# Performance work log

Measured on AMD Instinct MI355X. Metric: run time of the kernel, lower is better.

The kernel has to match this reference:

```python
import jax, jax.numpy as jnp
import numpy as np

B, S, D = 4, 2048, 1024
H, DK = 16, 64
NEG = -1e9


def setup_inputs() -> dict:
    key = jax.random.key(0)
    ks = jax.random.split(key, 6)
    hidden_states = jax.random.normal(ks[0], (B, S, D), dtype=jnp.float32)
    # evidence-constrained mask: causal mask plus random evidence restriction
    causal = jnp.tril(jnp.ones((S, S), dtype=bool))
    evid = jax.random.bernoulli(ks[1], 0.7, (S, S))
    allowed = causal & (evid | jnp.eye(S, dtype=bool))  # diag always allowed
    attention_mask = jnp.where(allowed, 0.0, NEG).astype(jnp.float32)
    scale = 0.02
    Wq = jax.random.normal(ks[2], (H * DK, D), dtype=jnp.float32) * scale
    Wk = jax.random.normal(ks[3], (H * DK, D), dtype=jnp.float32) * scale
    Wv = jax.random.normal(ks[4], (H * DK, D), dtype=jnp.float32) * scale
    Wo = jax.random.normal(ks[5], (D, H * DK), dtype=jnp.float32) * scale
    return {"hidden_states": hidden_states, "attention_mask": attention_mask,
            "Wq": Wq, "Wk": Wk, "Wv": Wv, "Wo": Wo}


def reference(hidden_states, attention_mask, Wq, Wk, Wv, Wo):
    b, s, _ = hidden_states.shape
    # nn.Linear(bias=False): y = x @ W.T ; reshape to (B,H,S,DK)
    def proj(x, W):
        y = jnp.einsum('bsd,ed->bse', x, W)
        return y.reshape(b, s, H, DK).transpose(0, 2, 1, 3)
    q = proj(hidden_states, Wq)
    k = proj(hidden_states, Wk)
    v = proj(hidden_states, Wv)
    logits = jnp.einsum('bhqd,bhkd->bhqk', q, k) / jnp.sqrt(jnp.float32(DK))
    logits = logits + attention_mask[None, None, :, :]
    attn = jax.nn.softmax(logits, axis=-1)
    ctx = jnp.einsum('bhqk,bhkd->bhqd', attn, v)
    ctx = ctx.transpose(0, 2, 1, 3).reshape(b, s, H * DK)
    out = jnp.einsum('bse,de->bsd', ctx, Wo)
    return out
```

## Files before the change

kernel.cpp:

```cpp
#include <hip/hip_runtime.h>
#include <hip/hip_bf16.h>
#include <math.h>

#define B_  4
#define S_  2048
#define D_  1024
#define H_  16
#define DK_ 64
#define M_  (B_*S_)
#define E_  (H_*DK_)
#define LOG2E  1.4426950408889634f
#define QSCALE 0.18033688011112042f

typedef short  bf16x8 __attribute__((ext_vector_type(8)));
typedef float  f32x4  __attribute__((ext_vector_type(4)));
typedef unsigned short u16;

__device__ __forceinline__ u16 f2b(float x) {
    __hip_bfloat16 h = __float2bfloat16(x);
    return *(u16*)&h;
}

__device__ __forceinline__ void async16(const u16* g, u16* l) {
    __builtin_amdgcn_global_load_lds(
        (const __attribute__((address_space(1))) unsigned int*)g,
        (__attribute__((address_space(3))) unsigned int*)l, 16, 0, 0);
}

#define XN8 (M_ * D_ / 8)
#define WN8 (E_ * D_ / 8)
__global__ __launch_bounds__(256)
void cvt_all(const float* __restrict__ X,
             const float* __restrict__ Wq, const float* __restrict__ Wk,
             const float* __restrict__ Wv, const float* __restrict__ Wo,
             u16* __restrict__ Xb,
             u16* __restrict__ Wqb, u16* __restrict__ Wkb,
             u16* __restrict__ Wvb, u16* __restrict__ Wob) {
    int idx = blockIdx.x * 256 + threadIdx.x;
    const float* s; u16* d; int off;
    if (idx < XN8) { s = X; d = Xb; off = idx; }
    else {
        int j = idx - XN8;
        int which = j / WN8; off = j - which * WN8;
        s = which == 0 ? Wq : which == 1 ? Wk : which == 2 ? Wv : Wo;
        d = which == 0 ? Wqb : which == 1 ? Wkb : which == 2 ? Wvb : Wob;
    }
    const float4* s4 = (const float4*)s;
    float4 a = s4[2 * off], b = s4[2 * off + 1];
    u16 o[8] = {f2b(a.x), f2b(a.y), f2b(a.z), f2b(a.w),
                f2b(b.x), f2b(b.y), f2b(b.z), f2b(b.w)};
    *(uint4*)(d + (size_t)8 * off) = *(const uint4*)o;
}

__device__ __forceinline__ void gemm_core(
    const u16* __restrict__ Ag, const u16* __restrict__ Bg, int K,
    int bm, int bn, u16* As, u16* Bs, f32x4 (&acc)[4][4])
{
    const int tid  = threadIdx.x;
    const int w    = tid >> 6, lane = tid & 63;
    const int l15  = lane & 15, quad = lane >> 4;
    const int wm   = (w >> 1) * 64, wn = (w & 1) * 64;
    const int srow = lane >> 3;
    const int sg   = (lane & 7) ^ srow;
    const int sx   = l15 & 7;

    for (int k0 = 0; k0 < K; k0 += 64) {
        __syncthreads();
        #pragma unroll
        for (int i = 0; i < 4; i++) {
            const int row = w * 32 + i * 8 + srow;
            async16(Ag + (size_t)(bm + row) * K + k0 + sg * 8,
                    As + (size_t)(w * 32 + i * 8) * 64);
            async16(Bg + (size_t)(bn + row) * K + k0 + sg * 8,
                    Bs + (size_t)(w * 32 + i * 8) * 64);
        }
        __syncthreads();

        #pragma unroll
        for (int s = 0; s < 2; s++) {
            bf16x8 af[4], bf[4];
            #pragma unroll
            for (int i = 0; i < 4; i++)
                af[i] = *(const bf16x8*)(As + (size_t)(wm + i * 16 + l15) * 64
                                            + (((s * 4 + quad) ^ sx) * 8));
            #pragma unroll
            for (int j = 0; j < 4; j++)
                bf[j] = *(const bf16x8*)(Bs + (size_t)(wn + j * 16 + l15) * 64
                                            + (((s * 4 + quad) ^ sx) * 8));
            #pragma unroll
            for (int i = 0; i < 4; i++)
                #pragma unroll
                for (int j = 0; j < 4; j++)
                    acc[i][j] = __builtin_amdgcn_mfma_f32_16x16x32_bf16(af[i], bf[j], acc[i][j], 0, 0, 0);
        }
    }
}

__global__ __launch_bounds__(256)
void gemm_qkv(const u16* __restrict__ Xb,
              const u16* __restrict__ Wqb, const u16* __restrict__ Wkb,
              const u16* __restrict__ Wvb,
              u16* __restrict__ Qm, u16* __restrict__ Km, u16* __restrict__ Vt)
{
    __shared__ u16 As[128 * 64];
    __shared__ u16 Bs[128 * 64];
    const int bm    = blockIdx.x * 128;
    const int nb    = blockIdx.y;
    const int which = nb >> 3;
    const int col0  = (nb & 7) * 128;
    const u16* Bg = which == 0 ? Wqb : which == 1 ? Wkb : Wvb;

    f32x4 acc[4][4] = {};
    gemm_core(Xb, Bg, D_, bm, col0, As, Bs, acc);

    const int tid = threadIdx.x;
    const int w   = tid >> 6, lane = tid & 63;
    const int l15 = lane & 15, quad = lane >> 4;
    const int wm  = (w >> 1) * 64, wn = (w & 1) * 64;

    if (which == 2) {
        #pragma unroll
        for (int i = 0; i < 4; i++)
            #pragma unroll
            for (int j = 0; j < 4; j++) {
                int c    = col0 + wn + j * 16 + l15;
                int tok0 = bm + wm + i * 16 + quad * 4;
                u16 pk[4] = {f2b(acc[i][j][0]), f2b(acc[i][j][1]),
                             f2b(acc[i][j][2]), f2b(acc[i][j][3])};
                size_t idx = (((size_t)((tok0 >> 11) * E_ + c)) << 11) + (tok0 & 2047);
                *(uint2*)(Vt + idx) = *(const uint2*)pk;
            }
    } else {
        u16* Cm = which == 0 ? Qm : Km;
        const float sc = which == 0 ? QSCALE : 1.0f;
        #pragma unroll
        for (int i = 0; i < 4; i++)
            #pragma unroll
            for (int j = 0; j < 4; j++)
                #pragma unroll
                for (int r = 0; r < 4; r++) {
                    int row = bm + wm + i * 16 + quad * 4 + r;
                    int c   = col0 + wn + j * 16 + l15;
                    Cm[(size_t)row * E_ + c] = f2b(acc[i][j][r] * sc);
                }
    }
}

__global__ __launch_bounds__(256)
void gemm_out(const u16* __restrict__ Cmx, const u16* __restrict__ Wob,
              float* __restrict__ out)
{
    __shared__ u16 As[128 * 64];
    __shared__ u16 Bs[128 * 64];
    const int bm = blockIdx.x * 128;
    const int bn = blockIdx.y * 128;

    f32x4 acc[4][4] = {};
    gemm_core(Cmx, Wob, E_, bm, bn, As, Bs, acc);

    const int tid = threadIdx.x;
    const int w   = tid >> 6, lane = tid & 63;
    const int l15 = lane & 15, quad = lane >> 4;
    const int wm  = (w >> 1) * 64, wn = (w & 1) * 64;
    #pragma unroll
    for (int i = 0; i < 4; i++)
        #pragma unroll
        for (int j = 0; j < 4; j++)
            #pragma unroll
            for (int r = 0; r < 4; r++)
                out[(size_t)(bm + wm + i * 16 + quad * 4 + r) * D_ + bn + wn + j * 16 + l15]
                    = acc[i][j][r];
}

__global__ __launch_bounds__(512)
void flash_attn(const u16* __restrict__ Q, const u16* __restrict__ Kc,
                const u16* __restrict__ Vt, const float* __restrict__ mask,
                u16* __restrict__ ctx)
{
    const int bh  = blockIdx.x;
    const int qt  = (gridDim.y - 1) - blockIdx.y;
    const int b   = bh >> 4, h = bh & 15;
    const int tid = threadIdx.x;
    const int w   = tid >> 6, lane = tid & 63;
    const int l15 = lane & 15, quad = lane >> 4;
    const int q0  = qt * 128;
    const int nkt = 2 * qt + 2;

    __shared__ u16 Ks[64 * 64];
    __shared__ u16 Vs[64 * 64];
    __shared__ u16 Ps[8][16 * 64];

    const u16* qb = Q + ((size_t)(b * S_ + q0 + w * 16 + l15)) * E_ + h * DK_;
    bf16x8 qf0 = *(const bf16x8*)(qb + quad * 8);
    bf16x8 qf1 = *(const bf16x8*)(qb + 32 + quad * 8);

    f32x4 acc[4] = {};
    float lsum = 0.f;

    const int sr = lane >> 3;
    const int sg = (lane & 7) ^ sr;
    const int sx = l15 & 7;
    u16* Pw = &Ps[w][0];
    const float* mpb = mask + (size_t)(q0 + w * 16 + l15) * S_ + quad * 4;

    for (int kt = 0; kt < nkt; ++kt) {
        const int k0 = kt * 64;

        float4 mk[4];
        #pragma unroll
        for (int t = 0; t < 4; t++) mk[t] = *(const float4*)(mpb + k0 + t * 16);

        __syncthreads();
        {
            const int row8 = w * 8;
            async16(Kc + ((size_t)(b * S_ + k0 + row8 + sr)) * E_ + h * DK_ + sg * 8,
                    Ks + row8 * 64);
            async16(Vt + ((size_t)(bh * DK_ + row8 + sr)) * S_ + k0 + sg * 8,
                    Vs + row8 * 64);
        }
        __syncthreads();

        f32x4 st[4] = {};
        #pragma unroll
        for (int t = 0; t < 4; t++) {
            bf16x8 kf0 = *(const bf16x8*)(Ks + (t * 16 + l15) * 64 + ((quad ^ sx) * 8));
            bf16x8 kf1 = *(const bf16x8*)(Ks + (t * 16 + l15) * 64 + (((4 + quad) ^ sx) * 8));
            st[t] = __builtin_amdgcn_mfma_f32_16x16x32_bf16(kf0, qf0, st[t], 0, 0, 0);
            st[t] = __builtin_amdgcn_mfma_f32_16x16x32_bf16(kf1, qf1, st[t], 0, 0, 0);
        }

        #pragma unroll
        for (int t = 0; t < 4; t++) {
            float p0 = exp2f(fmaf(mk[t].x, LOG2E, st[t][0]));
            float p1 = exp2f(fmaf(mk[t].y, LOG2E, st[t][1]));
            float p2 = exp2f(fmaf(mk[t].z, LOG2E, st[t][2]));
            float p3 = exp2f(fmaf(mk[t].w, LOG2E, st[t][3]));
            lsum += (p0 + p1) + (p2 + p3);
            u16 pk[4] = {f2b(p0), f2b(p1), f2b(p2), f2b(p3)};
            *(uint2*)(Pw + l15 * 64 + (((2 * t + (quad >> 1)) ^ sx) * 8) + (quad & 1) * 4)
                = *(const uint2*)pk;
        }

        #pragma unroll
        for (int sb = 0; sb < 2; sb++) {
            bf16x8 pf = *(const bf16x8*)(Pw + l15 * 64 + (((4 * sb + quad) ^ sx) * 8));
            #pragma unroll
            for (int nt = 0; nt < 4; nt++) {
                bf16x8 vf = *(const bf16x8*)(Vs + (nt * 16 + l15) * 64 + (((4 * sb + quad) ^ sx) * 8));
                acc[nt] = __builtin_amdgcn_mfma_f32_16x16x32_bf16(pf, vf, acc[nt], 0, 0, 0);
            }
        }
    }

    lsum += __shfl_xor(lsum, 16, 64);
    lsum += __shfl_xor(lsum, 32, 64);
    float linv = 1.0f / lsum;
    float ir[4];
    #pragma unroll
    for (int r = 0; r < 4; r++) ir[r] = __shfl(linv, quad * 4 + r, 16);
    #pragma unroll
    for (int r = 0; r < 4; r++) {
        size_t orow = ((size_t)(b * S_ + q0 + w * 16 + quad * 4 + r)) * E_ + h * DK_;
        #pragma unroll
        for (int nt = 0; nt < 4; nt++)
            ctx[orow + nt * 16 + l15] = f2b(acc[nt][r] * ir[r]);
    }
}

extern "C" void kernel_launch(void* const* d_in, const int* in_sizes, int n_in,
                              void* d_out, int out_size, void* d_ws, size_t ws_size,
                              hipStream_t stream) {
    const float* X    = (const float*)d_in[0];
    const float* mask = (const float*)d_in[1];
    const float* Wq   = (const float*)d_in[2];
    const float* Wk   = (const float*)d_in[3];
    const float* Wv   = (const float*)d_in[4];
    const float* Wo   = (const float*)d_in[5];
    float* out = (float*)d_out;

    char* p = (char*)d_ws;
    u16* Qm  = (u16*)p; p += (size_t)M_ * E_ * 2;
    u16* Km  = (u16*)p; p += (size_t)M_ * E_ * 2;
    u16* Vt  = (u16*)p; p += (size_t)M_ * E_ * 2;
    u16* Wqb = (u16*)p; p += (size_t)E_ * D_ * 2;
    u16* Wkb = (u16*)p; p += (size_t)E_ * D_ * 2;
    u16* Wvb = (u16*)p; p += (size_t)E_ * D_ * 2;
    u16* Wob = (u16*)p; p += (size_t)D_ * E_ * 2;
    u16* Xb  = (u16*)p;
    u16* Cm  = Xb;

    cvt_all<<<(XN8 + 4 * WN8 + 255) / 256, 256, 0, stream>>>(
        X, Wq, Wk, Wv, Wo, Xb, Wqb, Wkb, Wvb, Wob);

    gemm_qkv<<<dim3(M_ / 128, 24), 256, 0, stream>>>(Xb, Wqb, Wkb, Wvb, Qm, Km, Vt);

    flash_attn<<<dim3(B_ * H_, S_ / 128), 512, 0, stream>>>(Qm, Km, Vt, mask, Cm);

    gemm_out<<<dim3(M_ / 128, D_ / 128), 256, 0, stream>>>(Cm, Wob, out);
}
```

Measured before the change: 278.5 us.

## Add dedicated producer wave with double-buffered K/V tiles in flash attention

Adds a ninth wave to the attention block whose only job is issuing the async global-to-LDS loads of the next K/V tile. K and V are double-buffered in shared memory, so the loads can overlap the eight consumer waves' MFMA and softmax work, and each iteration needs one barrier instead of two. The trade-offs are that a single wave now issues all sixteen loads per tile, the block grows to 576 threads, and shared memory use rises, which may lower occupancy.

```diff
diff --git a/kernel.cpp b/kernel.cpp
--- a/kernel.cpp
+++ b/kernel.cpp
@@ -172,7 +172,7 @@
                     = acc[i][j][r];
 }
 
-__global__ __launch_bounds__(512)
+__global__ __launch_bounds__(576)
 void flash_attn(const u16* __restrict__ Q, const u16* __restrict__ Kc,
                 const u16* __restrict__ Vt, const float* __restrict__ mask,
                 u16* __restrict__ ctx)
@@ -186,84 +186,107 @@
     const int q0  = qt * 128;
     const int nkt = 2 * qt + 2;
 
-    __shared__ u16 Ks[64 * 64];
-    __shared__ u16 Vs[64 * 64];
+    __shared__ u16 Ks[2][64 * 64];
+    __shared__ u16 Vs[2][64 * 64];
     __shared__ u16 Ps[8][16 * 64];
-
-    const u16* qb = Q + ((size_t)(b * S_ + q0 + w * 16 + l15)) * E_ + h * DK_;
-    bf16x8 qf0 = *(const bf16x8*)(qb + quad * 8);
-    bf16x8 qf1 = *(const bf16x8*)(qb + 32 + quad * 8);
-
-    f32x4 acc[4] = {};
-    float lsum = 0.f;
 
     const int sr = lane >> 3;
     const int sg = (lane & 7) ^ sr;
     const int sx = l15 & 7;
-    u16* Pw = &Ps[w][0];
-    const float* mpb = mask + (size_t)(q0 + w * 16 + l15) * S_ + quad * 4;
+
+    const bool producer = (w == 8);
+
+    bf16x8 qf0 = {}, qf1 = {};
+    f32x4 acc[4] = {};
+    float lsum = 0.f;
+    u16* Pw = &Ps[w & 7][0];
+    const float* mpb = mask + (size_t)(q0 + (w & 7) * 16 + l15) * S_ + quad * 4;
+
+    if (!producer) {
+        const u16* qb = Q + ((size_t)(b * S_ + q0 + w * 16 + l15)) * E_ + h * DK_;
+        qf0 = *(const bf16x8*)(qb + quad * 8);
+        qf1 = *(const bf16x8*)(qb + 32 + quad * 8);
+    } else {
+        #pragma unroll
+        for (int i = 0; i < 8; i++) {
+            async16(Kc + ((size_t)(b * S_ + i * 8 + sr)) * E_ + h * DK_ + sg * 8,
+                    &Ks[0][(i * 8) * 64]);
+            async16(Vt + ((size_t)(bh * DK_ + i * 8 + sr)) * S_ + sg * 8,
+                    &Vs[0][(i * 8) * 64]);
+        }
+    }
+    __syncthreads();
 
     for (int kt = 0; kt < nkt; ++kt) {
-        const int k0 = kt * 64;
-
-        float4 mk[4];
-        #pragma unroll
-        for (int t = 0; t < 4; t++) mk[t] = *(const float4*)(mpb + k0 + t * 16);
+        const int buf = kt & 1;
+
+        if (producer) {
+            if (kt + 1 < nkt) {
+                const int k1 = (kt + 1) * 64, nb = buf ^ 1;
+                #pragma unroll
+                for (int i = 0; i < 8; i++) {
+                    async16(Kc + ((size_t)(b * S_ + k1 + i * 8 + sr)) * E_ + h * DK_ + sg * 8,
+                            &Ks[nb][(i * 8) * 64]);
+                    async16(Vt + ((size_t)(bh * DK_ + i * 8 + sr)) * S_ + k1 + sg * 8,
+                            &Vs[nb][(i * 8) * 64]);
+                }
+            }
+        } else {
+            const int k0 = kt * 64;
+
+            float4 mk[4];
+            #pragma unroll
+            for (int t = 0; t < 4; t++) mk[t] = *(const float4*)(mpb + k0 + t * 16);
+
+            f32x4 st[4] = {};
+            #pragma unroll
+            for (int t = 0; t < 4; t++) {
+                bf16x8 kf0 = *(const bf16x8*)(&Ks[buf][(t * 16 + l15) * 64 + ((quad ^ sx) * 8)]);
+                bf16x8 kf1 = *(const bf16x8*)(&Ks[buf][(t * 16 + l15) * 64 + (((4 + quad) ^ sx) * 8)]);
+                st[t] = __builtin_amdgcn_mfma_f32_16x16x32_bf16(kf0, qf0, st[t], 0, 0, 0);
+                st[t] = __builtin_amdgcn_mfma_f32_16x16x32_bf16(kf1, qf1, st[t], 0, 0, 0);
+            }
+
+            #pragma unroll
+            for (int t = 0; t < 4; t++) {
+                float p0 = exp2f(fmaf(mk[t].x, LOG2E, st[t][0]));
+                float p1 = exp2f(fmaf(mk[t].y, LOG2E, st[t][1]));
+                float p2 = exp2f(fmaf(mk[t].z, LOG2E, st[t][2]));
+                float p3 = exp2f(fmaf(mk[t].w, LOG2E, st[t][3]));
+                lsum += (p0 + p1) + (p2 + p3);
+                u16 pk[4] = {f2b(p0), f2b(p1), f2b(p2), f2b(p3)};
+                *(uint2*)(Pw + l15 * 64 + (((2 * t + (quad >> 1)) ^ sx) * 8) + (quad & 1) * 4)
+                    = *(const uint2*)pk;
+            }
+
+            #pragma unroll
+            for (int sb = 0; sb < 2; sb++) {
+                bf16x8 pf = *(const bf16x8*)(Pw + l15 * 64 + (((4 * sb + quad) ^ sx) * 8));
+                #pragma unroll
+                for (int nt = 0; nt < 4; nt++) {
+                    bf16x8 vf = *(const bf16x8*)(&Vs[buf][(nt * 16 + l15) * 64 + (((4 * sb + quad) ^ sx) * 8)]);
+                    acc[nt] = __builtin_amdgcn_mfma_f32_16x16x32_bf16(pf, vf, acc[nt], 0, 0, 0);
+                }
+            }
+        }
 
         __syncthreads();
-        {
-            const int row8 = w * 8;
-            async16(Kc + ((size_t)(b * S_ + k0 + row8 + sr)) * E_ + h * DK_ + sg * 8,
-                    Ks + row8 * 64);
-            async16(Vt + ((size_t)(bh * DK_ + row8 + sr)) * S_ + k0 + sg * 8,
-                    Vs + row8 * 64);
-        }
-        __syncthreads();
-
-        f32x4 st[4] = {};
-        #pragma unroll
-        for (int t = 0; t < 4; t++) {
-            bf16x8 kf0 = *(const bf16x8*)(Ks + (t * 16 + l15) * 64 + ((quad ^ sx) * 8));
-            bf16x8 kf1 = *(const bf16x8*)(Ks + (t * 16 + l15) * 64 + (((4 + quad) ^ sx) * 8));
-            st[t] = __builtin_amdgcn_mfma_f32_16x16x32_bf16(kf0, qf0, st[t], 0, 0, 0);
-            st[t] = __builtin_amdgcn_mfma_f32_16x16x32_bf16(kf1, qf1, st[t], 0, 0, 0);
-        }
-
-        #pragma unroll
-        for (int t = 0; t < 4; t++) {
-            float p0 = exp2f(fmaf(mk[t].x, LOG2E, st[t][0]));
-            float p1 = exp2f(fmaf(mk[t].y, LOG2E, st[t][1]));
-            float p2 = exp2f(fmaf(mk[t].z, LOG2E, st[t][2]));
-            float p3 = exp2f(fmaf(mk[t].w, LOG2E, st[t][3]));
-            lsum += (p0 + p1) + (p2 + p3);
-            u16 pk[4] = {f2b(p0), f2b(p1), f2b(p2), f2b(p3)};
-            *(uint2*)(Pw + l15 * 64 + (((2 * t + (quad >> 1)) ^ sx) * 8) + (quad & 1) * 4)
-                = *(const uint2*)pk;
-        }
-
-        #pragma unroll
-        for (int sb = 0; sb < 2; sb++) {
-            bf16x8 pf = *(const bf16x8*)(Pw + l15 * 64 + (((4 * sb + quad) ^ sx) * 8));
-            #pragma unroll
-            for (int nt = 0; nt < 4; nt++) {
-                bf16x8 vf = *(const bf16x8*)(Vs + (nt * 16 + l15) * 64 + (((4 * sb + quad) ^ sx) * 8));
-                acc[nt] = __builtin_amdgcn_mfma_f32_16x16x32_bf16(pf, vf, acc[nt], 0, 0, 0);
-            }
-        }
-    }
-
-    lsum += __shfl_xor(lsum, 16, 64);
-    lsum += __shfl_xor(lsum, 32, 64);
-    float linv = 1.0f / lsum;
-    float ir[4];
-    #pragma unroll
-    for (int r = 0; r < 4; r++) ir[r] = __shfl(linv, quad * 4 + r, 16);
-    #pragma unroll
-    for (int r = 0; r < 4; r++) {
-        size_t orow = ((size_t)(b * S_ + q0 + w * 16 + quad * 4 + r)) * E_ + h * DK_;
-        #pragma unroll
-        for (int nt = 0; nt < 4; nt++)
-            ctx[orow + nt * 16 + l15] = f2b(acc[nt][r] * ir[r]);
+    }
+
+    if (!producer) {
+        lsum += __shfl_xor(lsum, 16, 64);
+        lsum += __shfl_xor(lsum, 32, 64);
+        float linv = 1.0f / lsum;
+        float ir[4];
+        #pragma unroll
+        for (int r = 0; r < 4; r++) ir[r] = __shfl(linv, quad * 4 + r, 16);
+        #pragma unroll
+        for (int r = 0; r < 4; r++) {
+            size_t orow = ((size_t)(b * S_ + q0 + w * 16 + quad * 4 + r)) * E_ + h * DK_;
+            #pragma unroll
+            for (int nt = 0; nt < 4; nt++)
+                ctx[orow + nt * 16 + l15] = f2b(acc[nt][r] * ir[r]);
+        }
     }
 }
 
@@ -294,7 +317,7 @@
 
     gemm_qkv<<<dim3(M_ / 128, 24), 256, 0, stream>>>(Xb, Wqb, Wkb, Wvb, Qm, Km, Vt);
 
-    flash_attn<<<dim3(B_ * H_, S_ / 128), 512, 0, stream>>>(Qm, Km, Vt, mask, Cm);
+    flash_attn<<<dim3(B_ * H_, S_ / 128), 576, 0, stream>>>(Qm, Km, Vt, mask, Cm);
 
     gemm_out<<<dim3(M_ / 128, D_ / 128), 256, 0, stream>>>(Cm, Wob, out);
 }
```

Result: slower. 329.1 us (+18.1%).
